# Kernel tuning notes

Hardware: AMD Instinct MI355X
Metric: run time of the kernel (lower is better)

The kernel has to match this reference:

```python
import jax, jax.numpy as jnp
import numpy as np

# irrep blocks for 0e+1o+2e: dims 1, 3, 5 (total D=9)
BLOCKS = [(0, 1), (1, 4), (4, 9)]

def block_linear(x, W):
    # x: [N, C, 9], W: [3, C, C] -- e3nn Linear mixes channels within each irrep block
    outs = [jnp.einsum('ncd,cq->nqd', x[..., s:e], W[l]) for l, (s, e) in enumerate(BLOCKS)]
    return jnp.concatenate(outs, axis=-1)

def setup_inputs() -> dict:
    key = jax.random.key(0)
    ks = jax.random.split(key, 14)
    N, E, C, D, B, H, Z = 16384, 262144, 32, 9, 8, 64, 4
    inp = {
        'node_feats': jax.random.normal(ks[0], (N, C, D), jnp.float32),
        'node_attrs': jax.random.uniform(ks[1], (N, Z), jnp.float32),
        'edge_feats': jax.random.normal(ks[2], (E, B), jnp.float32),
        'edge_sh': jax.random.normal(ks[3], (E, D), jnp.float32),
        'cutoff': jax.random.uniform(ks[4], (E, 1), jnp.float32),
        # learned params
        'W_up': jax.random.normal(ks[5], (3, C, C), jnp.float32) / np.float32(np.sqrt(C)),
        'W1': jax.random.normal(ks[6], (B, H), jnp.float32) / np.float32(np.sqrt(B)),
        'W2': jax.random.normal(ks[7], (H, H), jnp.float32) / np.float32(np.sqrt(H)),
        'W3': jax.random.normal(ks[8], (H, C), jnp.float32) / np.float32(np.sqrt(H)),
        'W_lin': jax.random.normal(ks[9], (3, C, C), jnp.float32) / np.float32(np.sqrt(C)),
        'W_sc': jax.random.normal(ks[10], (Z, 3, C, C), jnp.float32) / np.float32(np.sqrt(C)),
        # fixed Clebsch-Gordan-like coupling tensor (constant structure of the TP)
        'CG': jax.random.normal(ks[11], (D, D, D), jnp.float32) / np.float32(D),
        'edge_src': jax.random.randint(ks[12], (E,), 0, N, jnp.int32),
        'edge_dst': jax.random.randint(ks[13], (E,), 0, N, jnp.int32),
    }
    return inp

def reference(node_feats, node_attrs, edge_feats, edge_sh, cutoff,
              W_up, W1, W2, W3, W_lin, W_sc, CG, edge_src, edge_dst):
    N = node_feats.shape[0]
    avg_num_neighbors = 16.0
    # linear_up: per-irrep channel mixing
    x = block_linear(node_feats, W_up)
    # radial MLP -> per-edge tensor-product weights, gated by cutoff
    h = jax.nn.silu(edge_feats @ W1)
    h = jax.nn.silu(h @ W2)
    w = (h @ W3) * cutoff  # [E, C]
    # gather source node feats, weighted equivariant tensor product per edge
    xs = x[edge_src]  # [E, C, D]
    m_ij = jnp.einsum('eci,ej,ijk,ec->eck', xs, edge_sh, CG, w)  # [E, C, D]
    # scatter-sum aggregation into destination nodes
    m_i = jax.ops.segment_sum(m_ij, edge_dst, num_segments=N)  # [N, C, D]
    # output linear + neighbor normalization
    m_i = block_linear(m_i, W_lin) / avg_num_neighbors
    # element-dependent self-connection from current message
    W_node = jnp.einsum('nz,zlcq->nlcq', node_attrs, W_sc)  # [N, 3, C, C]
    scs = jnp.concatenate(
        [jnp.einsum('ncd,ncq->nqd', m_i[..., s:e], W_node[:, l]) for l, (s, e) in enumerate(BLOCKS)],
        axis=-1)
    return (m_i, scs)
```

## Files before the change

kernel.cpp:

```cpp
#include <hip/hip_runtime.h>
#include <cstdint>

#define CC 32
#define DD 9
#define CD 288
#define BB 8
#define HH 64
#define ZZ 4
#define NB 8

typedef __attribute__((ext_vector_type(8))) short bf16x8;
typedef __attribute__((ext_vector_type(4))) float f32x4;
typedef __attribute__((ext_vector_type(2))) float f32x2;

__device__ __forceinline__ float silu_f(float v) {
  return v / (1.0f + __expf(-v));
}

__device__ __forceinline__ int blk_of(int d) { return d == 0 ? 0 : (d < 4 ? 1 : 2); }

__device__ __forceinline__ unsigned int f2bf(float f) {
  unsigned int u = __float_as_uint(f);
  return (u + 0x7fffu + ((u >> 16) & 1u)) >> 16;
}
__device__ __forceinline__ float bf_lo(unsigned int u) { return __uint_as_float(u << 16); }
__device__ __forceinline__ float bf_hi(unsigned int u) { return __uint_as_float(u & 0xffff0000u); }

__global__ __launch_bounds__(256) void k_zero(float* __restrict__ p, int n) {
  int i = blockIdx.x * 256 + threadIdx.x;
  if (i < n) p[i] = 0.0f;
}

__global__ __launch_bounds__(256) void k_hist(const int* __restrict__ edst,
                                              int* __restrict__ deg, int E) {
  int e = blockIdx.x * 256 + threadIdx.x;
  if (e < E) atomicAdd(&deg[edst[e]], 1);
}

__global__ __launch_bounds__(1024) void k_scan(const int* __restrict__ deg,
                                               int* __restrict__ offs,
                                               int* __restrict__ cursor, int N) {
  __shared__ int part[1024];
  int t = threadIdx.x;
  int chunk = (N + 1023) >> 10;
  int base = t * chunk;
  int lim = N - base; if (lim > chunk) lim = chunk; if (lim < 0) lim = 0;
  int s = 0;
  for (int i = 0; i < lim; ++i) s += deg[base + i];
  part[t] = s;
  __syncthreads();
  for (int off = 1; off < 1024; off <<= 1) {
    int v = part[t];
    int u = (t >= off) ? part[t - off] : 0;
    __syncthreads();
    part[t] = v + u;
    __syncthreads();
  }
  int run = (t == 0) ? 0 : part[t - 1];
  for (int i = 0; i < lim; ++i) {
    offs[base + i] = run;
    cursor[base + i] = run;
    run += deg[base + i];
  }
  if (t == 1023) offs[N] = run;
}

__global__ __launch_bounds__(256) void k_scatter(const int* __restrict__ edst,
                                                 const int* __restrict__ esrc,
                                                 const float* __restrict__ esh,
                                                 int* __restrict__ cursor,
                                                 int* __restrict__ eidx,
                                                 int* __restrict__ srcs,
                                                 unsigned int* __restrict__ esh_p, int E) {
  int e = blockIdx.x * 256 + threadIdx.x;
  if (e < E) {
    int d = edst[e];
    int pos = atomicAdd(&cursor[d], 1);
    eidx[pos] = e;
    srcs[pos] = esrc[e];
    const float* sp = esh + (size_t)e * 9;
    unsigned int* op = esh_p + (size_t)pos * 5;
#pragma unroll
    for (int jj = 0; jj < 5; ++jj) {
      unsigned int lo = f2bf(sp[2 * jj]);
      unsigned int hi = (jj < 4) ? f2bf(sp[2 * jj + 1]) : 0u;
      op[jj] = lo | (hi << 16);
    }
  }
}

__global__ __launch_bounds__(288) void k_linear_up(
    const float* __restrict__ nf, const float* __restrict__ Wup,
    unsigned int* __restrict__ x_p, int N) {
  __shared__ float snf[NB][DD * 36];
  __shared__ float sval[NB][DD][CC];
  int t = threadIdx.x;
  int g = t >> 5, q = t & 31;
  int tc = t / 9, td = t - tc * 9;
  int l0 = blk_of(g);
  float wcol[CC];
#pragma unroll
  for (int c = 0; c < CC; ++c) wcol[c] = Wup[l0 * 1024 + c * 32 + q];
  int n0 = blockIdx.x * NB;
#pragma unroll
  for (int nb = 0; nb < NB; ++nb) {
    if (n0 + nb < N) snf[nb][td * 36 + tc] = nf[(size_t)(n0 + nb) * CD + t];
  }
  __syncthreads();
#pragma unroll
  for (int nb = 0; nb < NB; ++nb) {
    if (n0 + nb >= N) break;
    const float4* rowp = (const float4*)(snf[nb] + g * 36);
    float a0 = 0.f, a1 = 0.f;
#pragma unroll
    for (int c4 = 0; c4 < 8; ++c4) {
      float4 b = rowp[c4];
      a0 += b.x * wcol[c4 * 4 + 0] + b.y * wcol[c4 * 4 + 1];
      a1 += b.z * wcol[c4 * 4 + 2] + b.w * wcol[c4 * 4 + 3];
    }
    sval[nb][g][q] = a0 + a1;
  }
  __syncthreads();
#pragma unroll
  for (int it = 0; it < 5; ++it) {
    int idx = it * 288 + t;
    if (idx < NB * 160) {
      int nb = idx / 160, r = idx - nb * 160;
      int p = r >> 5, c = r & 31;
      if (n0 + nb < N) {
        unsigned int lo = f2bf(sval[nb][2 * p][c]);
        unsigned int hi = (p < 4) ? f2bf(sval[nb][2 * p + 1][c]) : 0u;
        x_p[(size_t)(n0 + nb) * 160 + r] = lo | (hi << 16);
      }
    }
  }
}

__global__ __launch_bounds__(64) void k_mlp_mfma(
    const float* __restrict__ ef, const float* __restrict__ cut,
    const float* __restrict__ W1, const float* __restrict__ W2,
    const float* __restrict__ W3, const int* __restrict__ eidx,
    unsigned int* __restrict__ w_p, int E) {
  __shared__ ushort hbuf[4096];
  __shared__ ushort h2buf[4096];
  __shared__ float scut[64];
  int l = threadIdx.x;
  int h = l >> 4, li = l & 15;
  bf16x8 A2[4][2];
#pragma unroll
  for (int qm = 0; qm < 4; ++qm)
#pragma unroll
    for (int kb = 0; kb < 2; ++kb)
#pragma unroll
      for (int j = 0; j < 8; ++j)
        A2[qm][kb][j] = (short)f2bf(W2[(32 * kb + 8 * h + j) * HH + 16 * qm + li]);
  bf16x8 A3[2][2];
#pragma unroll
  for (int cm = 0; cm < 2; ++cm)
#pragma unroll
    for (int kb = 0; kb < 2; ++kb)
#pragma unroll
      for (int j = 0; j < 8; ++j)
        A3[cm][kb][j] = (short)f2bf(W3[(32 * kb + 8 * h + j) * CC + 16 * cm + li]);

  int ntile = E >> 6;
  for (int tile = blockIdx.x; tile < ntile; tile += gridDim.x) {
    int pos = tile * 64 + l;
    int eo = eidx[pos];
    const float4* efp = (const float4*)(ef + (size_t)eo * BB);
    float4 efa = efp[0];
    float4 efb = efp[1];
    scut[l] = cut[eo];
    float efv[BB] = {efa.x, efa.y, efa.z, efa.w, efb.x, efb.y, efb.z, efb.w};
#pragma unroll
    for (int g = 0; g < 8; ++g) {
      float hv[8];
#pragma unroll
      for (int jj = 0; jj < 8; ++jj) {
        int q = g * 8 + jj;
        float a = 0.f;
#pragma unroll
        for (int kin = 0; kin < BB; ++kin) a += efv[kin] * W1[kin * HH + q];
        hv[jj] = silu_f(a);
      }
      unsigned int d0 = f2bf(hv[0]) | (f2bf(hv[1]) << 16);
      unsigned int d1 = f2bf(hv[2]) | (f2bf(hv[3]) << 16);
      unsigned int d2 = f2bf(hv[4]) | (f2bf(hv[5]) << 16);
      unsigned int d3 = f2bf(hv[6]) | (f2bf(hv[7]) << 16);
      int F = ((l >> 4) * 2 + (g >> 2)) * 4 + (g & 3);
      *(uint4*)&hbuf[(F * 16 + li) * 8] = make_uint4(d0, d1, d2, d3);
    }
    f32x4 acc2[4][4];
#pragma unroll
    for (int qm = 0; qm < 4; ++qm)
#pragma unroll
      for (int nb = 0; nb < 4; ++nb) acc2[qm][nb] = (f32x4){0.f, 0.f, 0.f, 0.f};
#pragma unroll
    for (int nb = 0; nb < 4; ++nb)
#pragma unroll
      for (int kb = 0; kb < 2; ++kb) {
        int F = (nb * 2 + kb) * 4 + h;
        bf16x8 Bf = *(const bf16x8*)&hbuf[(F * 16 + li) * 8];
#pragma unroll
        for (int qm = 0; qm < 4; ++qm)
          acc2[qm][nb] = __builtin_amdgcn_mfma_f32_16x16x32_bf16(
              A2[qm][kb], Bf, acc2[qm][nb], 0, 0, 0);
      }
#pragma unroll
    for (int qm = 0; qm < 4; ++qm)
#pragma unroll
      for (int nb = 0; nb < 4; ++nb) {
        float v0 = silu_f(acc2[qm][nb][0]);
        float v1 = silu_f(acc2[qm][nb][1]);
        float v2 = silu_f(acc2[qm][nb][2]);
        float v3 = silu_f(acc2[qm][nb][3]);
        unsigned int lo = f2bf(v0) | (f2bf(v1) << 16);
        unsigned int hi = f2bf(v2) | (f2bf(v3) << 16);
        int G = (nb * 2 + (qm >> 1)) * 4 + ((2 * qm + (h >> 1)) & 3);
        *(uint2*)&h2buf[(G * 16 + li) * 8 + (h & 1) * 4] = make_uint2(lo, hi);
      }
    f32x4 acc3[2][4];
#pragma unroll
    for (int cm = 0; cm < 2; ++cm)
#pragma unroll
      for (int nb = 0; nb < 4; ++nb) acc3[cm][nb] = (f32x4){0.f, 0.f, 0.f, 0.f};
#pragma unroll
    for (int nb = 0; nb < 4; ++nb)
#pragma unroll
      for (int kb = 0; kb < 2; ++kb) {
        int G = (nb * 2 + kb) * 4 + h;
        bf16x8 Bf = *(const bf16x8*)&h2buf[(G * 16 + li) * 8];
#pragma unroll
        for (int cm = 0; cm < 2; ++cm)
          acc3[cm][nb] = __builtin_amdgcn_mfma_f32_16x16x32_bf16(
              A3[cm][kb], Bf, acc3[cm][nb], 0, 0, 0);
      }
#pragma unroll
    for (int nb = 0; nb < 4; ++nb) {
      float cv = scut[16 * nb + li];
#pragma unroll
      for (int cm = 0; cm < 2; ++cm) {
        unsigned int lo = f2bf(acc3[cm][nb][0] * cv) | (f2bf(acc3[cm][nb][1] * cv) << 16);
        unsigned int hi = f2bf(acc3[cm][nb][2] * cv) | (f2bf(acc3[cm][nb][3] * cv) << 16);
        *(uint2*)&w_p[(size_t)(tile * 64 + 16 * nb + li) * 16 + 8 * cm + 2 * h] =
            make_uint2(lo, hi);
      }
    }
  }
}

__global__ __launch_bounds__(256) void k_gather(
    const unsigned int* __restrict__ x_p, const unsigned int* __restrict__ w_p,
    const unsigned int* __restrict__ esh_p, const float* __restrict__ CG,
    const int* __restrict__ offs, const int* __restrict__ srcs,
    float* __restrict__ mpre, int N) {
  int wid = (blockIdx.x * 256 + threadIdx.x) >> 6;
  if (wid >= N) return;
  int lane = threadIdx.x & 63;
  int h = lane >> 5, c = lane & 31;
  int beg = offs[wid], end = offs[wid + 1];
  f32x2 Pp[36];
  float P8[9];
#pragma unroll
  for (int i = 0; i < 36; ++i) Pp[i] = (f32x2){0.f, 0.f};
#pragma unroll
  for (int i = 0; i < 9; ++i) P8[i] = 0.f;

  bool okc;
  unsigned int wu_c;
  unsigned int shd_c[5];
  unsigned int xd_c[5];
  {
    int p = beg + h;
    okc = p < end;
    int pp = okc ? p : beg;
    int s = srcs[pp];
    wu_c = w_p[(size_t)pp * 16 + (c >> 1)];
    const unsigned int* shp = esh_p + (size_t)pp * 5;
#pragma unroll
    for (int j = 0; j < 5; ++j) shd_c[j] = shp[j];
    const unsigned int* xp = x_p + (size_t)s * 160 + c;
    xd_c[0] = xp[0]; xd_c[1] = xp[32]; xd_c[2] = xp[64]; xd_c[3] = xp[96]; xd_c[4] = xp[128];
  }

  for (int p0 = beg; p0 < end; p0 += 2) {
    int pn = p0 + 2 + h;
    bool okn = pn < end;
    int ppn = okn ? pn : beg;
    int s_n = srcs[ppn];
    unsigned int wu_n = w_p[(size_t)ppn * 16 + (c >> 1)];
    unsigned int shd_n[5];
    {
      const unsigned int* shp = esh_p + (size_t)ppn * 5;
#pragma unroll
      for (int j = 0; j < 5; ++j) shd_n[j] = shp[j];
    }
    unsigned int xd_n[5];
    {
      const unsigned int* xp = x_p + (size_t)s_n * 160 + c;
      xd_n[0] = xp[0]; xd_n[1] = xp[32]; xd_n[2] = xp[64]; xd_n[3] = xp[96]; xd_n[4] = xp[128];
    }
    float wc = okc ? ((c & 1) ? bf_hi(wu_c) : bf_lo(wu_c)) : 0.f;
    f32x2 sh2[4];
    sh2[0] = (f32x2){bf_lo(shd_c[0]), bf_hi(shd_c[0])};
    sh2[1] = (f32x2){bf_lo(shd_c[1]), bf_hi(shd_c[1])};
    sh2[2] = (f32x2){bf_lo(shd_c[2]), bf_hi(shd_c[2])};
    sh2[3] = (f32x2){bf_lo(shd_c[3]), bf_hi(shd_c[3])};
    float sh8 = bf_lo(shd_c[4]);
    float xs[DD];
    xs[0] = bf_lo(xd_c[0]); xs[1] = bf_hi(xd_c[0]);
    xs[2] = bf_lo(xd_c[1]); xs[3] = bf_hi(xd_c[1]);
    xs[4] = bf_lo(xd_c[2]); xs[5] = bf_hi(xd_c[2]);
    xs[6] = bf_lo(xd_c[3]); xs[7] = bf_hi(xd_c[3]);
    xs[8] = bf_lo(xd_c[4]);
#pragma unroll
    for (int i = 0; i < DD; ++i) {
      float t = wc * xs[i];
      f32x2 t2 = (f32x2){t, t};
#pragma unroll
      for (int jp = 0; jp < 4; ++jp) Pp[i * 4 + jp] = t2 * sh2[jp] + Pp[i * 4 + jp];
      P8[i] += t * sh8;
    }
    okc = okn;
    wu_c = wu_n;
#pragma unroll
    for (int j = 0; j < 5; ++j) { shd_c[j] = shd_n[j]; xd_c[j] = xd_n[j]; }
  }

  f32x2 m2[4];
  float m8 = 0.f;
#pragma unroll
  for (int kp = 0; kp < 4; ++kp) m2[kp] = (f32x2){0.f, 0.f};
#pragma unroll
  for (int i = 0; i < DD; ++i) {
#pragma unroll
    for (int j = 0; j < DD; ++j) {
      float p = (j < 8) ? ((j & 1) ? Pp[i * 4 + (j >> 1)].y : Pp[i * 4 + (j >> 1)].x)
                        : P8[i];
      f32x2 p2 = (f32x2){p, p};
      const float* cgr = CG + i * 81 + j * DD;
#pragma unroll
      for (int kp = 0; kp < 4; ++kp) {
        f32x2 cg2 = (f32x2){cgr[2 * kp], cgr[2 * kp + 1]};
        m2[kp] = p2 * cg2 + m2[kp];
      }
      m8 += p * cgr[8];
    }
  }
  float m[DD];
  m[0] = m2[0].x; m[1] = m2[0].y;
  m[2] = m2[1].x; m[3] = m2[1].y;
  m[4] = m2[2].x; m[5] = m2[2].y;
  m[6] = m2[3].x; m[7] = m2[3].y;
  m[8] = m8;
#pragma unroll
  for (int k = 0; k < DD; ++k) m[k] += __shfl_xor(m[k], 32);
  if (h == 0) {
    float* mp = mpre + (size_t)wid * CD + c;
#pragma unroll
    for (int k = 0; k < DD; ++k) mp[k * 32] = m[k];
  }
}

__global__ __launch_bounds__(288, 1) void k_out(
    const float* __restrict__ attrs, const float* __restrict__ Wlin,
    const float* __restrict__ Wsc,
    float* __restrict__ out1, float* __restrict__ out2, int N) {
  __shared__ float smp[NB][CD];
  __shared__ float smt[NB][CD];
  __shared__ float sres1[NB * CD];
  __shared__ float sres2[NB * CD];
  int t = threadIdx.x;
  int g = t >> 5, q = t & 31;
  int l0 = blk_of(g);
  float wl[CC];
#pragma unroll
  for (int c = 0; c < CC; ++c) wl[c] = Wlin[l0 * 1024 + c * 32 + q];
  float ws0[CC], ws1[CC], ws2[CC], ws3[CC];
#pragma unroll
  for (int c = 0; c < CC; ++c) {
    ws0[c] = Wsc[0 * 3072 + l0 * 1024 + c * 32 + q];
    ws1[c] = Wsc[1 * 3072 + l0 * 1024 + c * 32 + q];
    ws2[c] = Wsc[2 * 3072 + l0 * 1024 + c * 32 + q];
    ws3[c] = Wsc[3 * 3072 + l0 * 1024 + c * 32 + q];
  }
  int nbat = (N + NB - 1) / NB;
  int b = blockIdx.x;
  float r[NB];
  if (b < nbat) {
#pragma unroll
    for (int nb = 0; nb < NB; ++nb) r[nb] = out2[(size_t)(b * NB + nb) * CD + t];
  }
  for (; b < nbat; b += gridDim.x) {
    int n0 = b * NB;
    __syncthreads();
#pragma unroll
    for (int nb = 0; nb < NB; ++nb) smp[nb][t] = r[nb];
    float4 av[NB];
#pragma unroll
    for (int nb = 0; nb < NB; ++nb) av[nb] = ((const float4*)attrs)[n0 + nb];
    __syncthreads();
    int b2 = b + gridDim.x;
    if (b2 < nbat) {
#pragma unroll
      for (int nb = 0; nb < NB; ++nb) r[nb] = out2[(size_t)(b2 * NB + nb) * CD + t];
    }
#pragma unroll
    for (int nb = 0; nb < NB; ++nb) {
      const float4* rowp = (const float4*)(smp[nb] + g * 32);
      float b0 = 0.f, b1 = 0.f;
#pragma unroll
      for (int c4 = 0; c4 < 8; ++c4) {
        float4 bb = rowp[c4];
        b0 += bb.x * wl[c4 * 4 + 0] + bb.y * wl[c4 * 4 + 1];
        b1 += bb.z * wl[c4 * 4 + 2] + bb.w * wl[c4 * 4 + 3];
      }
      float v = (b0 + b1) * (1.0f / 16.0f);
      smt[nb][t] = v;
      sres1[nb * CD + q * DD + g] = v;
    }
    __syncthreads();
#pragma unroll
    for (int nb = 0; nb < NB; ++nb) {
      const float4* rowp = (const float4*)(smt[nb] + g * 32);
      float z0 = 0.f, z1 = 0.f, z2 = 0.f, z3 = 0.f;
#pragma unroll
      for (int c4 = 0; c4 < 8; ++c4) {
        float4 bb = rowp[c4];
#pragma unroll
        for (int j = 0; j < 4; ++j) {
          float bv = (j == 0) ? bb.x : (j == 1) ? bb.y : (j == 2) ? bb.z : bb.w;
          int c = c4 * 4 + j;
          z0 += bv * ws0[c];
          z1 += bv * ws1[c];
          z2 += bv * ws2[c];
          z3 += bv * ws3[c];
        }
      }
      float4 a = av[nb];
      sres2[nb * CD + q * DD + g] = a.x * z0 + a.y * z1 + a.z * z2 + a.w * z3;
    }
    __syncthreads();
#pragma unroll
    for (int rr = 0; rr < (NB * 72) / 288; ++rr) {
      int s = rr * 288 + t;
      int nb = s / 72, idx = s - nb * 72;
      ((float4*)(out1 + (size_t)(n0 + nb) * CD))[idx] = ((const float4*)sres1)[s];
      ((float4*)(out2 + (size_t)(n0 + nb) * CD))[idx] = ((const float4*)sres2)[s];
    }
  }
}

extern "C" void kernel_launch(void* const* d_in, const int* in_sizes, int n_in,
                              void* d_out, int out_size, void* d_ws, size_t ws_size,
                              hipStream_t stream) {
  const float* nf    = (const float*)d_in[0];
  const float* attrs = (const float*)d_in[1];
  const float* ef    = (const float*)d_in[2];
  const float* esh   = (const float*)d_in[3];
  const float* cutv  = (const float*)d_in[4];
  const float* Wup   = (const float*)d_in[5];
  const float* W1    = (const float*)d_in[6];
  const float* W2    = (const float*)d_in[7];
  const float* W3    = (const float*)d_in[8];
  const float* Wlin  = (const float*)d_in[9];
  const float* Wsc   = (const float*)d_in[10];
  const float* CG    = (const float*)d_in[11];
  const int* esrc    = (const int*)d_in[12];
  const int* edst    = (const int*)d_in[13];
  int N = in_sizes[0] / CD;
  int E = in_sizes[12];
  float* out1 = (float*)d_out;
  float* out2 = out1 + (size_t)N * CD;

  unsigned int* x_p   = (unsigned int*)d_ws;
  unsigned int* w_p   = x_p + (size_t)N * 160;
  unsigned int* esh_p = w_p + (size_t)E * 16;
  int* deg     = (int*)(esh_p + (size_t)E * 5);
  int* offs    = deg + N;
  int* cursor  = offs + N + 1;
  int* eidx    = cursor + N;
  int* srcs    = eidx + E;

  int nblk = (N + NB - 1) / NB;
  k_zero<<<(N + 255) / 256, 256, 0, stream>>>((float*)deg, N);
  k_hist<<<(E + 255) / 256, 256, 0, stream>>>(edst, deg, E);
  k_scan<<<1, 1024, 0, stream>>>(deg, offs, cursor, N);
  k_scatter<<<(E + 255) / 256, 256, 0, stream>>>(edst, esrc, esh, cursor, eidx, srcs, esh_p, E);
  k_linear_up<<<nblk, 288, 0, stream>>>(nf, Wup, x_p, N);
  k_mlp_mfma<<<4096, 64, 0, stream>>>(ef, cutv, W1, W2, W3, eidx, w_p, E);
  k_gather<<<(N + 3) / 4, 256, 0, stream>>>(x_p, w_p, esh_p, CG, offs, srcs, out2, N);
  k_out<<<512, 288, 0, stream>>>(attrs, Wlin, Wsc, out1, out2, N);
}
```

Measured before the change: 235.6 us.

## Pad packed edge SH to 8 words, swap zero kernel for memset, double k_out grid

Packed bf16 edge spherical harmonics now use a stride of 8 words per edge instead of 5, so the gather kernel can fetch them with one 16-byte vector load plus one scalar load. The custom zeroing kernel is replaced with hipMemsetAsync, and the output kernel grid goes from 512 to 1024 blocks. The padding raises workspace size and scatter write footprint, and the changes are otherwise unrelated.

```diff
diff --git a/kernel.cpp b/kernel.cpp
--- a/kernel.cpp
+++ b/kernel.cpp
@@ -25,11 +25,6 @@
 }
 __device__ __forceinline__ float bf_lo(unsigned int u) { return __uint_as_float(u << 16); }
 __device__ __forceinline__ float bf_hi(unsigned int u) { return __uint_as_float(u & 0xffff0000u); }
-
-__global__ __launch_bounds__(256) void k_zero(float* __restrict__ p, int n) {
-  int i = blockIdx.x * 256 + threadIdx.x;
-  if (i < n) p[i] = 0.0f;
-}
 
 __global__ __launch_bounds__(256) void k_hist(const int* __restrict__ edst,
                                               int* __restrict__ deg, int E) {
@@ -79,7 +74,7 @@
     eidx[pos] = e;
     srcs[pos] = esrc[e];
     const float* sp = esh + (size_t)e * 9;
-    unsigned int* op = esh_p + (size_t)pos * 5;
+    unsigned int* op = esh_p + (size_t)pos * 8;
 #pragma unroll
     for (int jj = 0; jj < 5; ++jj) {
       unsigned int lo = f2bf(sp[2 * jj]);
@@ -268,7 +263,7 @@
 
   bool okc;
   unsigned int wu_c;
-  unsigned int shd_c[5];
+  uint4 shv_c; unsigned int sh4_c;
   unsigned int xd_c[5];
   {
     int p = beg + h;
@@ -276,9 +271,9 @@
     int pp = okc ? p : beg;
     int s = srcs[pp];
     wu_c = w_p[(size_t)pp * 16 + (c >> 1)];
-    const unsigned int* shp = esh_p + (size_t)pp * 5;
-#pragma unroll
-    for (int j = 0; j < 5; ++j) shd_c[j] = shp[j];
+    const unsigned int* shp = esh_p + (size_t)pp * 8;
+    shv_c = *(const uint4*)shp;
+    sh4_c = shp[4];
     const unsigned int* xp = x_p + (size_t)s * 160 + c;
     xd_c[0] = xp[0]; xd_c[1] = xp[32]; xd_c[2] = xp[64]; xd_c[3] = xp[96]; xd_c[4] = xp[128];
   }
@@ -289,12 +284,9 @@
     int ppn = okn ? pn : beg;
     int s_n = srcs[ppn];
     unsigned int wu_n = w_p[(size_t)ppn * 16 + (c >> 1)];
-    unsigned int shd_n[5];
-    {
-      const unsigned int* shp = esh_p + (size_t)ppn * 5;
-#pragma unroll
-      for (int j = 0; j < 5; ++j) shd_n[j] = shp[j];
-    }
+    const unsigned int* shp_n = esh_p + (size_t)ppn * 8;
+    uint4 shv_n = *(const uint4*)shp_n;
+    unsigned int sh4_n = shp_n[4];
     unsigned int xd_n[5];
     {
       const unsigned int* xp = x_p + (size_t)s_n * 160 + c;
@@ -302,11 +294,11 @@
     }
     float wc = okc ? ((c & 1) ? bf_hi(wu_c) : bf_lo(wu_c)) : 0.f;
     f32x2 sh2[4];
-    sh2[0] = (f32x2){bf_lo(shd_c[0]), bf_hi(shd_c[0])};
-    sh2[1] = (f32x2){bf_lo(shd_c[1]), bf_hi(shd_c[1])};
-    sh2[2] = (f32x2){bf_lo(shd_c[2]), bf_hi(shd_c[2])};
-    sh2[3] = (f32x2){bf_lo(shd_c[3]), bf_hi(shd_c[3])};
-    float sh8 = bf_lo(shd_c[4]);
+    sh2[0] = (f32x2){bf_lo(shv_c.x), bf_hi(shv_c.x)};
+    sh2[1] = (f32x2){bf_lo(shv_c.y), bf_hi(shv_c.y)};
+    sh2[2] = (f32x2){bf_lo(shv_c.z), bf_hi(shv_c.z)};
+    sh2[3] = (f32x2){bf_lo(shv_c.w), bf_hi(shv_c.w)};
+    float sh8 = bf_lo(sh4_c);
     float xs[DD];
     xs[0] = bf_lo(xd_c[0]); xs[1] = bf_hi(xd_c[0]);
     xs[2] = bf_lo(xd_c[1]); xs[3] = bf_hi(xd_c[1]);
@@ -323,8 +315,9 @@
     }
     okc = okn;
     wu_c = wu_n;
-#pragma unroll
-    for (int j = 0; j < 5; ++j) { shd_c[j] = shd_n[j]; xd_c[j] = xd_n[j]; }
+    shv_c = shv_n; sh4_c = sh4_n;
+#pragma unroll
+    for (int j = 0; j < 5; ++j) xd_c[j] = xd_n[j];
   }
 
   f32x2 m2[4];
@@ -476,19 +469,19 @@
   unsigned int* x_p   = (unsigned int*)d_ws;
   unsigned int* w_p   = x_p + (size_t)N * 160;
   unsigned int* esh_p = w_p + (size_t)E * 16;
-  int* deg     = (int*)(esh_p + (size_t)E * 5);
+  int* deg     = (int*)(esh_p + (size_t)E * 8);
   int* offs    = deg + N;
   int* cursor  = offs + N + 1;
   int* eidx    = cursor + N;
   int* srcs    = eidx + E;
 
   int nblk = (N + NB - 1) / NB;
-  k_zero<<<(N + 255) / 256, 256, 0, stream>>>((float*)deg, N);
+  hipMemsetAsync(deg, 0, (size_t)N * sizeof(int), stream);
   k_hist<<<(E + 255) / 256, 256, 0, stream>>>(edst, deg, E);
   k_scan<<<1, 1024, 0, stream>>>(deg, offs, cursor, N);
   k_scatter<<<(E + 255) / 256, 256, 0, stream>>>(edst, esrc, esh, cursor, eidx, srcs, esh_p, E);
   k_linear_up<<<nblk, 288, 0, stream>>>(nf, Wup, x_p, N);
   k_mlp_mfma<<<4096, 64, 0, stream>>>(ef, cutv, W1, W2, W3, eidx, w_p, E);
   k_gather<<<(N + 3) / 4, 256, 0, stream>>>(x_p, w_p, esh_p, CG, offs, srcs, out2, N);
-  k_out<<<512, 288, 0, stream>>>(attrs, Wlin, Wsc, out1, out2, N);
-}
+  k_out<<<1024, 288, 0, stream>>>(attrs, Wlin, Wsc, out1, out2, N);
+}
```

Result: no change. 240.1 us (+1.9%).
